# Kernel tuning notes

Measured on AMD Instinct MI355X. Metric: run time of the kernel, lower is better.

The kernel has to match this reference:

```python
import jax, jax.numpy as jnp
import numpy as np

B, N, C_IN = 4, 4096, 64
DIM = 64
NKP = 15
K = 32               # neighbor_limits
CONV_RADIUS = 0.1 * 2.0   # conv_radius * rigid_scale (is_deform=False)
KERNEL_RADIUS = 0.12
RECEP = 1.2          # kernel_point_receptive_radius
TRANS_DIM = 128
INF = 1000000.0


def _square_distance(src, dst):
    # src [B,N,3], dst [B,M,3] -> [B,N,M]
    d = -2.0 * jnp.einsum('bnc,bmc->bnm', src, dst)
    d = d + jnp.sum(src * src, -1)[:, :, None]
    d = d + jnp.sum(dst * dst, -1)[:, None, :]
    return d


def _query_ball(xyz, radius):
    # xyz [B,N,3] -> neighbor idx [B,N,K]; out-of-radius mapped to N (shadow)
    n = xyz.shape[1]
    sq = _square_distance(xyz, xyz)
    idx = jnp.broadcast_to(jnp.arange(n, dtype=jnp.int32), sq.shape)
    idx = jnp.where(sq > radius * radius, n, idx)
    idx = jnp.sort(idx, axis=-1)[:, :, :K]
    return idx


def _index_points(points_bcn, idx, pad_val):
    # points [B,C,N], idx [B,N,K] -> [B,N,K,C]; index N hits shadow row = pad_val
    p = jnp.transpose(points_bcn, (0, 2, 1))          # [B,N,C]
    shadow = jnp.full((p.shape[0], 1, p.shape[2]), pad_val, p.dtype)
    p = jnp.concatenate([p, shadow], axis=1)          # [B,N+1,C]
    b_idx = jnp.arange(p.shape[0])[:, None, None]
    return p[b_idx, idx]                              # [B,N,K,C]


def setup_inputs() -> dict:
    key = jax.random.key(0)
    ks = jax.random.split(key, 12)
    pos = jax.random.uniform(ks[0], (B, 3, N), dtype=jnp.float32)
    feat = jax.random.normal(ks[1], (B, C_IN, N), dtype=jnp.float32)
    # kernel points: center point at origin, rest inside kernel_radius ball ('center' mode)
    kp_rest = jax.random.uniform(ks[2], (3, NKP - 1), minval=-KERNEL_RADIUS,
                                 maxval=KERNEL_RADIUS, dtype=jnp.float32)
    kp_pos = jnp.concatenate([jnp.zeros((3, 1), jnp.float32), kp_rest], axis=1)  # [3,NKP]
    s = 0.05
    cb_w = jax.random.normal(ks[3], (DIM, C_IN), jnp.float32) * s
    cb_b = jax.random.normal(ks[4], (DIM,), jnp.float32) * s
    kp_weight = jax.random.normal(ks[5], (NKP, DIM, DIM), jnp.float32) * s
    kp_bias = jax.random.normal(ks[6], (DIM,), jnp.float32) * s
    ce_w = jax.random.normal(ks[7], (C_IN, DIM), jnp.float32) * s
    ce_b = jax.random.normal(ks[8], (C_IN,), jnp.float32) * s
    f1_w = jax.random.normal(ks[9], (2 * DIM, 2 * DIM), jnp.float32) * s
    f1_b = jnp.zeros((2 * DIM,), jnp.float32)
    f2_w = jax.random.normal(ks[10], (TRANS_DIM, 2 * DIM), jnp.float32) * s
    f2_b = jnp.zeros((TRANS_DIM,), jnp.float32)
    return dict(pos=pos, feat=feat, kp_pos=kp_pos, cb_w=cb_w, cb_b=cb_b,
                kp_weight=kp_weight, kp_bias=kp_bias, ce_w=ce_w, ce_b=ce_b,
                f1_w=f1_w, f1_b=f1_b, f2_w=f2_w, f2_b=f2_b)


def reference(pos, feat, kp_pos, cb_w, cb_b, kp_weight, kp_bias, ce_w, ce_b,
              f1_w, f1_b, f2_w, f2_b):
    xyz = jnp.transpose(jax.lax.stop_gradient(pos), (0, 2, 1))       # [B,N,3]
    neighbor_idx = _query_ball(xyz, CONV_RADIUS)                     # [B,N,K]
    # NOTE: with is_deform=False the original code does NOT subtract the center
    # position; rel_neighbor_pos is the absolute gathered positions.
    neighbor_pos = jnp.transpose(_index_points(pos, neighbor_idx, INF),
                                 (0, 3, 1, 2))                        # [B,3,N,K]
    feat0 = jnp.einsum('oc,bcn->bon', cb_w, feat) + cb_b[None, :, None]
    neighbor_feat = _index_points(feat0, neighbor_idx, 0.0)           # [B,N,K,DIM]

    kp_pos_deform = kp_pos.reshape(1, 3, 1, NKP) + 0.0                # offset = 0
    diff = neighbor_pos[..., None] - kp_pos_deform[:, :, :, None, :]  # [B,3,N,K,NKP]
    sq_d = jnp.sum(diff * diff, axis=1)                               # [B,N,K,NKP]
    w = jnp.clip(1.0 - jnp.sqrt(sq_d) / RECEP, 0.0)                   # [B,N,K,NKP]
    w = jnp.transpose(w, (0, 1, 3, 2))                                # [B,N,NKP,K]
    weighted = jnp.einsum('bnpk,bnkc->bnpc', w, neighbor_feat)        # [B,N,NKP,DIM]
    out = jnp.einsum('bnpc,pcd->bnd', weighted, kp_weight) + kp_bias  # [B,N,DIM]
    out = jax.nn.relu(jnp.transpose(out, (0, 2, 1)))                  # [B,DIM,N]
    out = jax.nn.relu(jnp.einsum('oc,bcn->bon', ce_w, out)
                      + ce_b[None, :, None] + feat)                   # [B,C_IN,N]

    fuse_in = jnp.concatenate(
        [jnp.transpose(weighted, (0, 3, 1, 2)),                       # [B,DIM,N,NKP]
         jnp.broadcast_to(out[..., None], (B, DIM, N, NKP))], axis=1) # [B,2DIM,N,NKP]
    h = jax.nn.relu(jnp.einsum('oc,bcnk->bonk', f1_w, fuse_in)
                    + f1_b[None, :, None, None])
    fuse = jax.nn.relu(jnp.einsum('oc,bcnk->bonk', f2_w, h)
                       + f2_b[None, :, None, None])                   # [B,TRANS_DIM,N,NKP]
    return out, kp_pos_deform, fuse
```

## Files before the change

kernel.cpp:

```cpp
#include <hip/hip_runtime.h>
#include <hip/hip_bf16.h>
#include <stdint.h>

#define NPTS 4096
#define NB   4
#define KNN  32
#define NKPT 15

#define OFF_IDX      0ULL
#define OFF_FEAT0    2097152ULL
#define OFF_WEIGHTED 6292480ULL
#define OFF_ROUT0    37749760ULL
#define OFF_W1P      41944064ULL
#define OFF_W2P      41976832ULL
#define OFF_KPWP     42009600ULL

#define OUT_OFF_OUT  0
#define OUT_OFF_KP   1048576
#define OUT_OFF_FUSE 1048621

#define SBU(u) ((u) ^ (((u) >> 3) & 7))

typedef __attribute__((ext_vector_type(8))) short short8v;
typedef __attribute__((ext_vector_type(4))) float f32x4;

__device__ __forceinline__ unsigned short bf16b(float f) {
  __hip_bfloat16 h = __float2bfloat16(f);
  return *(unsigned short*)&h;
}
__device__ __forceinline__ unsigned pkbf(float lo, float hi) {
  return (unsigned)bf16b(lo) | ((unsigned)bf16b(hi) << 16);
}

__global__ __launch_bounds__(256) void k0_init(const float* __restrict__ f1_w,
                                               const float* __restrict__ f2_w,
                                               const float* __restrict__ kpw,
                                               const float* __restrict__ kp_pos,
                                               unsigned short* __restrict__ w1p,
                                               unsigned short* __restrict__ w2p,
                                               unsigned short* __restrict__ kpwp,
                                               float* __restrict__ feat0,
                                               float* __restrict__ out_kp) {
  int t = blockIdx.x * 256 + threadIdx.x;
  if (t < 32768) {
    const int w = t >> 14;
    const int i = t & 16383;
    const int j = i & 7, l = (i >> 3) & 63, kc = (i >> 9) & 3, ot = i >> 11;
    const int o = ot * 16 + (l & 15);
    const int k = kc * 32 + (l >> 4) * 8 + j;
    const float* src = w ? f2_w : f1_w;
    unsigned short* dst = w ? w2p : w1p;
    dst[i] = bf16b(src[o * 128 + k]);
    return;
  }
  t -= 32768;
  if (t < 61440) {
    const int j = t & 7, l = (t >> 3) & 63, nt = (t >> 9) & 3, kc = t >> 11;
    const int k = kc * 32 + (l >> 4) * 8 + j;
    const int d = nt * 16 + (l & 15);
    kpwp[t] = bf16b(kpw[(size_t)k * 64 + d]);
    return;
  }
  t -= 61440;
  if (t < NB * 64) { int b = t >> 6, d = t & 63; feat0[((size_t)b * (NPTS + 1) + NPTS) * 64 + d] = 0.f; return; }
  t -= NB * 64;
  if (t < 45) out_kp[t] = kp_pos[t];
}

__global__ __launch_bounds__(256) void k1_neigh(const float* __restrict__ pos,
                                                int* __restrict__ idx_ws) {
  const int w = threadIdx.x >> 6, lane = threadIdx.x & 63;
  const int pt = blockIdx.x * 4 + w;
  const int b = pt >> 12, n = pt & 4095;
  const float* px = pos + (size_t)b * 3 * NPTS;
  const double x0 = (double)px[n], y0 = (double)px[NPTS + n], z0 = (double)px[2 * NPTS + n];
  const double ssrc = x0 * x0 + y0 * y0 + z0 * z0;
  const double RAD = 0.1 * 2.0;
  const double R2 = RAD * RAD;
  int cnt = 0;
  int* op = idx_ws + (size_t)pt * KNN;
  for (int ch = 0; ch < 64; ++ch) {
    const int j = ch * 64 + lane;
    const double xj = (double)px[j], yj = (double)px[NPTS + j], zj = (double)px[2 * NPTS + j];
    const double dot  = x0 * xj + y0 * yj + z0 * zj;
    const double sdst = xj * xj + yj * yj + zj * zj;
    const double sq = -2.0 * dot + ssrc + sdst;
    const bool keep = !(sq > R2);
    const unsigned long long m = __ballot(keep);
    if (keep) {
      const int p = cnt + (int)__popcll(m & ((1ULL << lane) - 1ULL));
      if (p < KNN) op[p] = j;
    }
    cnt += (int)__popcll(m);
    if (cnt >= KNN) break;
  }
  const int s = cnt + lane;
  if (s < KNN) op[s] = NPTS;
}

__global__ __launch_bounds__(256) void k2_feat0(const float* __restrict__ feat,
                                                const float* __restrict__ cb_w,
                                                const float* __restrict__ cb_b,
                                                float* __restrict__ feat0) {
  __shared__ float cbt[64 * 65];
  const int t = threadIdx.x;
  #pragma unroll
  for (int q = 0; q < 16; ++q) {
    const int idx = q * 256 + t;
    const int d = idx >> 6, c = idx & 63;
    cbt[c * 65 + d] = cb_w[idx];
  }
  __syncthreads();
  const int ptl = t >> 6, d = t & 63;
  const int pt = blockIdx.x * 4 + ptl;
  const int b = pt >> 12, n = pt & 4095;
  const float* fp = feat + (size_t)b * 64 * NPTS + n;
  float acc = 0.f;
  #pragma unroll
  for (int c = 0; c < 64; ++c) acc = fmaf(cbt[c * 65 + d], fp[(size_t)c * NPTS], acc);
  acc += cb_b[d];
  feat0[((size_t)b * (NPTS + 1) + n) * 64 + d] = acc;
}

__global__ __launch_bounds__(64) void k3_weighted(const float* __restrict__ pos,
                                                  const int* __restrict__ idx_ws,
                                                  const float* __restrict__ feat0,
                                                  const float* __restrict__ kp_pos,
                                                  unsigned short* __restrict__ wbf) {
  __shared__ int   nidx[KNN];
  __shared__ float npx[KNN], npy[KNN], npz[KNN];
  __shared__ float kp[48];
  __shared__ float wl[KNN * 16];
  const int lane = threadIdx.x;
  const int pt = blockIdx.x;
  const int b = pt >> 12;
  if (lane < 45) kp[lane] = kp_pos[lane];
  if (lane < KNN) {
    const int ki = idx_ws[(size_t)pt * KNN + lane];
    nidx[lane] = ki;
    const bool v = ki < NPTS;
    const float* px = pos + (size_t)b * 3 * NPTS;
    npx[lane] = v ? px[ki] : 1000000.0f;
    npy[lane] = v ? px[NPTS + ki] : 1000000.0f;
    npz[lane] = v ? px[2 * NPTS + ki] : 1000000.0f;
  }
  __syncthreads();
  #pragma unroll
  for (int r = 0; r < 8; ++r) {
    const int i = r * 64 + lane;
    const int k = i >> 4, p = i & 15;
    float wv = 0.f;
    if (p < 15) {
      const float dx = npx[k] - kp[p];
      const float dy = npy[k] - kp[15 + p];
      const float dz = npz[k] - kp[30 + p];
      const float d2 = dx * dx + dy * dy + dz * dz;
      wv = fmaxf(1.0f - sqrtf(d2) / 1.2f, 0.f);
    }
    wl[i] = wv;
  }
  __syncthreads();
  float acc[16];
  #pragma unroll
  for (int p = 0; p < 16; ++p) acc[p] = 0.f;
  const float* f0 = feat0 + (size_t)b * (NPTS + 1) * 64 + lane;
  for (int k = 0; k < KNN; ++k) {
    const float f = f0[(size_t)nidx[k] * 64];
    #pragma unroll
    for (int q = 0; q < 4; ++q) {
      const float4 w4 = *(const float4*)&wl[k * 16 + q * 4];
      acc[q * 4 + 0] = fmaf(w4.x, f, acc[q * 4 + 0]);
      acc[q * 4 + 1] = fmaf(w4.y, f, acc[q * 4 + 1]);
      acc[q * 4 + 2] = fmaf(w4.z, f, acc[q * 4 + 2]);
      acc[q * 4 + 3] = fmaf(w4.w, f, acc[q * 4 + 3]);
    }
  }
  unsigned short* wp = wbf + (size_t)pt * NKPT * 64 + lane;
  #pragma unroll
  for (int p = 0; p < 15; ++p) wp[(size_t)p * 64] = bf16b(acc[p]);
}

__global__ __launch_bounds__(64) void k4_kpconv(const unsigned short* __restrict__ wbf,
                                                const unsigned short* __restrict__ kpwp,
                                                const float* __restrict__ kp_bias,
                                                float* __restrict__ rout0) {
  const int lane = threadIdx.x;
  const int m0 = blockIdx.x * 16;
  const short8v* kf = (const short8v*)kpwp;
  f32x4 acc[4];
  #pragma unroll
  for (int nt = 0; nt < 4; ++nt) acc[nt] = (f32x4){0.f, 0.f, 0.f, 0.f};
  const unsigned short* ap = wbf + (size_t)(m0 + (lane & 15)) * 960 + (lane >> 4) * 8;
  #pragma unroll 6
  for (int kc = 0; kc < 30; ++kc) {
    const short8v a = *(const short8v*)&ap[kc * 32];
    #pragma unroll
    for (int nt = 0; nt < 4; ++nt)
      acc[nt] = __builtin_amdgcn_mfma_f32_16x16x32_bf16(a, kf[(kc * 4 + nt) * 64 + lane], acc[nt], 0, 0, 0);
  }
  const int row = m0 + (lane >> 4) * 4;
  #pragma unroll
  for (int nt = 0; nt < 4; ++nt) {
    const int d = nt * 16 + (lane & 15);
    const float bv = kp_bias[d];
    #pragma unroll
    for (int r = 0; r < 4; ++r)
      rout0[(size_t)(row + r) * 64 + d] = fmaxf(acc[nt][r] + bv, 0.f);
  }
}

__global__ __launch_bounds__(256) void k5_out(const float* __restrict__ rout0,
                                              const float* __restrict__ ce_w,
                                              const float* __restrict__ ce_b,
                                              const float* __restrict__ feat,
                                              float* __restrict__ out) {
  __shared__ float r0[64 * 65];
  __shared__ float cwt[64 * 64];
  const int t = threadIdx.x;
  const int b = blockIdx.x >> 6;
  const int n0 = (blockIdx.x & 63) * 64;
  #pragma unroll
  for (int q = 0; q < 16; ++q) {
    const int idx = q * 256 + t;
    const int rr = idx >> 6, c = idx & 63;
    r0[rr * 65 + c] = rout0[((size_t)b * 4096 + n0 + rr) * 64 + c];
    cwt[idx] = ce_w[(idx & 63) * 64 + (idx >> 6)];
  }
  __syncthreads();
  const int nl = t & 63, og = t >> 6;
  float acc[16];
  #pragma unroll
  for (int j = 0; j < 16; ++j) acc[j] = 0.f;
  for (int c = 0; c < 64; ++c) {
    const float x = r0[nl * 65 + c];
    #pragma unroll
    for (int q = 0; q < 4; ++q) {
      const float4 w4 = *(const float4*)&cwt[c * 64 + og * 16 + q * 4];
      acc[q * 4 + 0] = fmaf(w4.x, x, acc[q * 4 + 0]);
      acc[q * 4 + 1] = fmaf(w4.y, x, acc[q * 4 + 1]);
      acc[q * 4 + 2] = fmaf(w4.z, x, acc[q * 4 + 2]);
      acc[q * 4 + 3] = fmaf(w4.w, x, acc[q * 4 + 3]);
    }
  }
  #pragma unroll
  for (int q = 0; q < 4; ++q) {
    const float4 cb4 = *(const float4*)&ce_b[og * 16 + q * 4];
    const float cbv[4] = {cb4.x, cb4.y, cb4.z, cb4.w};
    #pragma unroll
    for (int j = 0; j < 4; ++j) {
      const int o = og * 16 + q * 4 + j;
      const float fv = feat[((size_t)b * 64 + o) * 4096 + n0 + nl];
      out[((size_t)b * 64 + o) * 4096 + n0 + nl] = fmaxf((acc[q * 4 + j] + cbv[j]) + fv, 0.f);
    }
  }
}

__global__ __launch_bounds__(256, 2) void k6_fuse(const unsigned short* __restrict__ wbf,
                                                  const float* __restrict__ outp,
                                                  const unsigned short* __restrict__ w1p,
                                                  const float* __restrict__ f1_b,
                                                  const unsigned short* __restrict__ w2p,
                                                  const float* __restrict__ f2_b,
                                                  float* __restrict__ fuse) {
  __shared__ __attribute__((aligned(16))) unsigned short SB[16384];
  __shared__ float outS[64 * 12];
  const int t = threadIdx.x;
  const int blk = blockIdx.x;
  const int b = blk / 480;
  const int ml0 = (blk - b * 480) * 128;
  const size_t M0 = (size_t)blk * 128;
  const int wv = t >> 6, lane = t & 63;
  const short8v* w1f = (const short8v*)w1p;
  const short8v* w2f = (const short8v*)w2p;

  short8v w1r[32];
  #pragma unroll
  for (int i = 0; i < 32; ++i) w1r[i] = w1f[i * 64 + lane];

  const int nmin = ml0 / 15;
  #pragma unroll
  for (int q = 0; q < 3; ++q) {
    const int i = q * 256 + t;
    const int c2 = i / 12, nn = i - c2 * 12;
    int n = nmin + nn;
    if (n > 4095) n = 4095;
    outS[i] = outp[((size_t)b * 64 + c2) * 4096 + n];
  }
  #pragma unroll
  for (int q = 0; q < 4; ++q) {
    const int chunk = q * 256 + t;
    const int m = chunk >> 3, a = chunk & 7;
    const uint4 pk = *(const uint4*)&wbf[(M0 + m) * 64 + a * 8];
    const int kc = a >> 2, hi = a & 3;
    const int u = ((m >> 4) * 4 + kc) * 64 + hi * 16 + (m & 15);
    *(uint4*)&SB[SBU(u) * 8] = pk;
  }
  __syncthreads();
  #pragma unroll
  for (int q = 0; q < 4; ++q) {
    const int chunk = q * 256 + t;
    const int m = chunk >> 3, a = chunk & 7;
    const int dn = (ml0 + m) / 15 - nmin;
    float v[8];
    #pragma unroll
    for (int i = 0; i < 8; ++i) v[i] = outS[(a * 8 + i) * 12 + dn];
    const int c0 = 64 + a * 8;
    const int kc = c0 >> 5, hi = (c0 >> 3) & 3;
    const int u = ((m >> 4) * 4 + kc) * 64 + hi * 16 + (m & 15);
    uint4 pk;
    pk.x = pkbf(v[0], v[1]); pk.y = pkbf(v[2], v[3]);
    pk.z = pkbf(v[4], v[5]); pk.w = pkbf(v[6], v[7]);
    *(uint4*)&SB[SBU(u) * 8] = pk;
  }
  __syncthreads();

  short8v xf[8];
  #pragma unroll
  for (int mt = 0; mt < 2; ++mt)
    #pragma unroll
    for (int kc = 0; kc < 4; ++kc) {
      const int u = ((wv * 2 + mt) * 4 + kc) * 64 + lane;
      xf[mt * 4 + kc] = *(const short8v*)&SB[SBU(u) * 8];
    }

  f32x4 acc[8][2];
  #pragma unroll
  for (int ot = 0; ot < 8; ++ot) {
    acc[ot][0] = (f32x4){0.f, 0.f, 0.f, 0.f};
    acc[ot][1] = (f32x4){0.f, 0.f, 0.f, 0.f};
  }
  #pragma unroll
  for (int kc = 0; kc < 4; ++kc) {
    #pragma unroll
    for (int ot = 0; ot < 8; ++ot) {
      acc[ot][0] = __builtin_amdgcn_mfma_f32_16x16x32_bf16(w1r[ot * 4 + kc], xf[kc],     acc[ot][0], 0, 0, 0);
      acc[ot][1] = __builtin_amdgcn_mfma_f32_16x16x32_bf16(w1r[ot * 4 + kc], xf[4 + kc], acc[ot][1], 0, 0, 0);
    }
  }
  short8v w2r[32];
  #pragma unroll
  for (int i = 0; i < 32; ++i) w2r[i] = w2f[i * 64 + lane];

  const int rb = (lane >> 4) * 4;
  #pragma unroll
  for (int ot = 0; ot < 8; ++ot) {
    const int o0 = ot * 16 + rb;
    const float4 b1 = *(const float4*)&f1_b[o0];
    const int kc = o0 >> 5, hi = (o0 >> 3) & 3, j0 = o0 & 7;
    #pragma unroll
    for (int mt = 0; mt < 2; ++mt) {
      const f32x4 h = acc[ot][mt];
      const float h0 = fmaxf(h[0] + b1.x, 0.f);
      const float h1 = fmaxf(h[1] + b1.y, 0.f);
      const float h2 = fmaxf(h[2] + b1.z, 0.f);
      const float h3 = fmaxf(h[3] + b1.w, 0.f);
      const int u = ((wv * 2 + mt) * 4 + kc) * 64 + hi * 16 + (lane & 15);
      uint2 pk;
      pk.x = pkbf(h0, h1);
      pk.y = pkbf(h2, h3);
      *(uint2*)&SB[SBU(u) * 8 + j0] = pk;
    }
  }
  short8v hf[8];
  #pragma unroll
  for (int mt = 0; mt < 2; ++mt)
    #pragma unroll
    for (int kc = 0; kc < 4; ++kc) {
      const int u = ((wv * 2 + mt) * 4 + kc) * 64 + lane;
      hf[mt * 4 + kc] = *(const short8v*)&SB[SBU(u) * 8];
    }
  #pragma unroll
  for (int ot = 0; ot < 8; ++ot) {
    acc[ot][0] = (f32x4){0.f, 0.f, 0.f, 0.f};
    acc[ot][1] = (f32x4){0.f, 0.f, 0.f, 0.f};
  }
  #pragma unroll
  for (int kc = 0; kc < 4; ++kc) {
    #pragma unroll
    for (int ot = 0; ot < 8; ++ot) {
      acc[ot][0] = __builtin_amdgcn_mfma_f32_16x16x32_bf16(w2r[ot * 4 + kc], hf[kc],     acc[ot][0], 0, 0, 0);
      acc[ot][1] = __builtin_amdgcn_mfma_f32_16x16x32_bf16(w2r[ot * 4 + kc], hf[4 + kc], acc[ot][1], 0, 0, 0);
    }
  }
  float* fp0 = fuse + (size_t)b * 128 * 61440 + ml0 + wv * 32 + (lane & 15);
  #pragma unroll
  for (int ot = 0; ot < 8; ++ot) {
    const int o0 = ot * 16 + rb;
    const float4 b2 = *(const float4*)&f2_b[o0];
    const float bv[4] = {b2.x, b2.y, b2.z, b2.w};
    #pragma unroll
    for (int mt = 0; mt < 2; ++mt) {
      const f32x4 vacc = acc[ot][mt];
      #pragma unroll
      for (int r = 0; r < 4; ++r)
        fp0[(size_t)(o0 + r) * 61440 + mt * 16] = fmaxf(vacc[r] + bv[r], 0.f);
    }
  }
}

extern "C" void kernel_launch(void* const* d_in, const int* in_sizes, int n_in,
                              void* d_out, int out_size, void* d_ws, size_t ws_size,
                              hipStream_t stream) {
  const float* pos     = (const float*)d_in[0];
  const float* feat    = (const float*)d_in[1];
  const float* kp_pos  = (const float*)d_in[2];
  const float* cb_w    = (const float*)d_in[3];
  const float* cb_b    = (const float*)d_in[4];
  const float* kpw     = (const float*)d_in[5];
  const float* kp_bias = (const float*)d_in[6];
  const float* ce_w    = (const float*)d_in[7];
  const float* ce_b    = (const float*)d_in[8];
  const float* f1_w    = (const float*)d_in[9];
  const float* f1_b    = (const float*)d_in[10];
  const float* f2_w    = (const float*)d_in[11];
  const float* f2_b    = (const float*)d_in[12];
  float* out = (float*)d_out;
  char* ws = (char*)d_ws;
  int*   idx_ws   = (int*)(ws + OFF_IDX);
  float* feat0    = (float*)(ws + OFF_FEAT0);
  unsigned short* wbf  = (unsigned short*)(ws + OFF_WEIGHTED);
  float* rout0    = (float*)(ws + OFF_ROUT0);
  unsigned short* w1p  = (unsigned short*)(ws + OFF_W1P);
  unsigned short* w2p  = (unsigned short*)(ws + OFF_W2P);
  unsigned short* kpwp = (unsigned short*)(ws + OFF_KPWP);

  k0_init<<<370, 256, 0, stream>>>(f1_w, f2_w, kpw, kp_pos, w1p, w2p, kpwp, feat0,
                                   out + OUT_OFF_KP);
  k1_neigh<<<4096, 256, 0, stream>>>(pos, idx_ws);
  k2_feat0<<<4096, 256, 0, stream>>>(feat, cb_w, cb_b, feat0);
  k3_weighted<<<16384, 64, 0, stream>>>(pos, idx_ws, feat0, kp_pos, wbf);
  k4_kpconv<<<1024, 64, 0, stream>>>(wbf, kpwp, kp_bias, rout0);
  k5_out<<<256, 256, 0, stream>>>(rout0, ce_w, ce_b, feat, out + OUT_OFF_OUT);
  k6_fuse<<<1920, 256, 0, stream>>>(wbf, out + OUT_OFF_OUT, w1p, f1_b, w2p, f2_b,
                                    out + OUT_OFF_FUSE);
}
```

Baseline: 156.5 us.

## Merge setup kernels, fuse kpconv with output, precompute broadcast half of fuse MLP

```diff
diff --git a/kernel.cpp b/kernel.cpp
--- a/kernel.cpp
+++ b/kernel.cpp
@@ -10,10 +10,10 @@
 #define OFF_IDX      0ULL
 #define OFF_FEAT0    2097152ULL
 #define OFF_WEIGHTED 6292480ULL
-#define OFF_ROUT0    37749760ULL
-#define OFF_W1P      41944064ULL
-#define OFF_W2P      41976832ULL
-#define OFF_KPWP     42009600ULL
+#define OFF_HO       37749760ULL
+#define OFF_W1P      46138368ULL
+#define OFF_W2P      46171136ULL
+#define OFF_KPWP     46203904ULL
 
 #define OUT_OFF_OUT  0
 #define OUT_OFF_KP   1048576
@@ -32,16 +32,73 @@
   return (unsigned)bf16b(lo) | ((unsigned)bf16b(hi) << 16);
 }
 
-__global__ __launch_bounds__(256) void k0_init(const float* __restrict__ f1_w,
-                                               const float* __restrict__ f2_w,
-                                               const float* __restrict__ kpw,
-                                               const float* __restrict__ kp_pos,
-                                               unsigned short* __restrict__ w1p,
-                                               unsigned short* __restrict__ w2p,
-                                               unsigned short* __restrict__ kpwp,
-                                               float* __restrict__ feat0,
-                                               float* __restrict__ out_kp) {
-  int t = blockIdx.x * 256 + threadIdx.x;
+__global__ __launch_bounds__(256) void k012(const float* __restrict__ pos,
+                                            const float* __restrict__ feat,
+                                            const float* __restrict__ cb_w,
+                                            const float* __restrict__ cb_b,
+                                            const float* __restrict__ f1_w,
+                                            const float* __restrict__ f2_w,
+                                            const float* __restrict__ kpw,
+                                            const float* __restrict__ kp_pos,
+                                            int* __restrict__ idx_ws,
+                                            float* __restrict__ feat0,
+                                            unsigned short* __restrict__ w1p,
+                                            unsigned short* __restrict__ w2p,
+                                            unsigned short* __restrict__ kpwp,
+                                            float* __restrict__ out_kp) {
+  __shared__ float cbt[64 * 65];
+  const int blk = blockIdx.x;
+  if (blk < 4096) {
+    const int w = threadIdx.x >> 6, lane = threadIdx.x & 63;
+    const int pt = blk * 4 + w;
+    const int b = pt >> 12, n = pt & 4095;
+    const float* px = pos + (size_t)b * 3 * NPTS;
+    const double x0 = (double)px[n], y0 = (double)px[NPTS + n], z0 = (double)px[2 * NPTS + n];
+    const double ssrc = x0 * x0 + y0 * y0 + z0 * z0;
+    const double RAD = 0.1 * 2.0;
+    const double R2 = RAD * RAD;
+    int cnt = 0;
+    int* op = idx_ws + (size_t)pt * KNN;
+    for (int ch = 0; ch < 64; ++ch) {
+      const int j = ch * 64 + lane;
+      const double xj = (double)px[j], yj = (double)px[NPTS + j], zj = (double)px[2 * NPTS + j];
+      const double dot  = x0 * xj + y0 * yj + z0 * zj;
+      const double sdst = xj * xj + yj * yj + zj * zj;
+      const double sq = -2.0 * dot + ssrc + sdst;
+      const bool keep = !(sq > R2);
+      const unsigned long long m = __ballot(keep);
+      if (keep) {
+        const int p = cnt + (int)__popcll(m & ((1ULL << lane) - 1ULL));
+        if (p < KNN) op[p] = j;
+      }
+      cnt += (int)__popcll(m);
+      if (cnt >= KNN) break;
+    }
+    const int s = cnt + lane;
+    if (s < KNN) op[s] = NPTS;
+    return;
+  }
+  if (blk < 8192) {
+    const int t = threadIdx.x;
+    #pragma unroll
+    for (int q = 0; q < 16; ++q) {
+      const int idx = q * 256 + t;
+      const int d = idx >> 6, c = idx & 63;
+      cbt[c * 65 + d] = cb_w[idx];
+    }
+    __syncthreads();
+    const int ptl = t >> 6, d = t & 63;
+    const int pt = (blk - 4096) * 4 + ptl;
+    const int b = pt >> 12, n = pt & 4095;
+    const float* fp = feat + (size_t)b * 64 * NPTS + n;
+    float acc = 0.f;
+    #pragma unroll
+    for (int c = 0; c < 64; ++c) acc = fmaf(cbt[c * 65 + d], fp[(size_t)c * NPTS], acc);
+    acc += cb_b[d];
+    feat0[((size_t)b * (NPTS + 1) + n) * 64 + d] = acc;
+    return;
+  }
+  int t = (blk - 8192) * 256 + threadIdx.x;
   if (t < 32768) {
     const int w = t >> 14;
     const int i = t & 16383;
@@ -65,61 +122,6 @@
   if (t < NB * 64) { int b = t >> 6, d = t & 63; feat0[((size_t)b * (NPTS + 1) + NPTS) * 64 + d] = 0.f; return; }
   t -= NB * 64;
   if (t < 45) out_kp[t] = kp_pos[t];
-}
-
-__global__ __launch_bounds__(256) void k1_neigh(const float* __restrict__ pos,
-                                                int* __restrict__ idx_ws) {
-  const int w = threadIdx.x >> 6, lane = threadIdx.x & 63;
-  const int pt = blockIdx.x * 4 + w;
-  const int b = pt >> 12, n = pt & 4095;
-  const float* px = pos + (size_t)b * 3 * NPTS;
-  const double x0 = (double)px[n], y0 = (double)px[NPTS + n], z0 = (double)px[2 * NPTS + n];
-  const double ssrc = x0 * x0 + y0 * y0 + z0 * z0;
-  const double RAD = 0.1 * 2.0;
-  const double R2 = RAD * RAD;
-  int cnt = 0;
-  int* op = idx_ws + (size_t)pt * KNN;
-  for (int ch = 0; ch < 64; ++ch) {
-    const int j = ch * 64 + lane;
-    const double xj = (double)px[j], yj = (double)px[NPTS + j], zj = (double)px[2 * NPTS + j];
-    const double dot  = x0 * xj + y0 * yj + z0 * zj;
-    const double sdst = xj * xj + yj * yj + zj * zj;
-    const double sq = -2.0 * dot + ssrc + sdst;
-    const bool keep = !(sq > R2);
-    const unsigned long long m = __ballot(keep);
-    if (keep) {
-      const int p = cnt + (int)__popcll(m & ((1ULL << lane) - 1ULL));
-      if (p < KNN) op[p] = j;
-    }
-    cnt += (int)__popcll(m);
-    if (cnt >= KNN) break;
-  }
-  const int s = cnt + lane;
-  if (s < KNN) op[s] = NPTS;
-}
-
-__global__ __launch_bounds__(256) void k2_feat0(const float* __restrict__ feat,
-                                                const float* __restrict__ cb_w,
-                                                const float* __restrict__ cb_b,
-                                                float* __restrict__ feat0) {
-  __shared__ float cbt[64 * 65];
-  const int t = threadIdx.x;
-  #pragma unroll
-  for (int q = 0; q < 16; ++q) {
-    const int idx = q * 256 + t;
-    const int d = idx >> 6, c = idx & 63;
-    cbt[c * 65 + d] = cb_w[idx];
-  }
-  __syncthreads();
-  const int ptl = t >> 6, d = t & 63;
-  const int pt = blockIdx.x * 4 + ptl;
-  const int b = pt >> 12, n = pt & 4095;
-  const float* fp = feat + (size_t)b * 64 * NPTS + n;
-  float acc = 0.f;
-  #pragma unroll
-  for (int c = 0; c < 64; ++c) acc = fmaf(cbt[c * 65 + d], fp[(size_t)c * NPTS], acc);
-  acc += cb_b[d];
-  feat0[((size_t)b * (NPTS + 1) + n) * 64 + d] = acc;
 }
 
 __global__ __launch_bounds__(64) void k3_weighted(const float* __restrict__ pos,
@@ -180,16 +182,33 @@
   for (int p = 0; p < 15; ++p) wp[(size_t)p * 64] = bf16b(acc[p]);
 }
 
-__global__ __launch_bounds__(64) void k4_kpconv(const unsigned short* __restrict__ wbf,
-                                                const unsigned short* __restrict__ kpwp,
-                                                const float* __restrict__ kp_bias,
-                                                float* __restrict__ rout0) {
-  const int lane = threadIdx.x;
-  const int m0 = blockIdx.x * 16;
+__global__ __launch_bounds__(256) void k45(const unsigned short* __restrict__ wbf,
+                                           const unsigned short* __restrict__ kpwp,
+                                           const float* __restrict__ kp_bias,
+                                           const float* __restrict__ ce_w,
+                                           const float* __restrict__ ce_b,
+                                           const float* __restrict__ feat,
+                                           const unsigned short* __restrict__ w1p,
+                                           const float* __restrict__ f1_b,
+                                           float* __restrict__ out,
+                                           float* __restrict__ hO) {
+  __shared__ float r0[64 * 65];
+  __shared__ float cwt[64 * 64];
+  __shared__ unsigned short outT[64 * 74];
+  const int t = threadIdx.x;
+  const int b = blockIdx.x >> 6;
+  const int n0 = (blockIdx.x & 63) * 64;
+  const int wv = t >> 6, lane = t & 63;
+  #pragma unroll
+  for (int q = 0; q < 16; ++q) {
+    const int idx = q * 256 + t;
+    cwt[idx] = ce_w[(idx & 63) * 64 + (idx >> 6)];
+  }
   const short8v* kf = (const short8v*)kpwp;
   f32x4 acc[4];
   #pragma unroll
   for (int nt = 0; nt < 4; ++nt) acc[nt] = (f32x4){0.f, 0.f, 0.f, 0.f};
+  const int m0 = b * 4096 + n0 + wv * 16;
   const unsigned short* ap = wbf + (size_t)(m0 + (lane & 15)) * 960 + (lane >> 4) * 8;
   #pragma unroll 6
   for (int kc = 0; kc < 30; ++kc) {
@@ -198,48 +217,29 @@
     for (int nt = 0; nt < 4; ++nt)
       acc[nt] = __builtin_amdgcn_mfma_f32_16x16x32_bf16(a, kf[(kc * 4 + nt) * 64 + lane], acc[nt], 0, 0, 0);
   }
-  const int row = m0 + (lane >> 4) * 4;
+  const int rl = wv * 16 + (lane >> 4) * 4;
   #pragma unroll
   for (int nt = 0; nt < 4; ++nt) {
     const int d = nt * 16 + (lane & 15);
     const float bv = kp_bias[d];
     #pragma unroll
     for (int r = 0; r < 4; ++r)
-      rout0[(size_t)(row + r) * 64 + d] = fmaxf(acc[nt][r] + bv, 0.f);
-  }
-}
-
-__global__ __launch_bounds__(256) void k5_out(const float* __restrict__ rout0,
-                                              const float* __restrict__ ce_w,
-                                              const float* __restrict__ ce_b,
-                                              const float* __restrict__ feat,
-                                              float* __restrict__ out) {
-  __shared__ float r0[64 * 65];
-  __shared__ float cwt[64 * 64];
-  const int t = threadIdx.x;
-  const int b = blockIdx.x >> 6;
-  const int n0 = (blockIdx.x & 63) * 64;
-  #pragma unroll
-  for (int q = 0; q < 16; ++q) {
-    const int idx = q * 256 + t;
-    const int rr = idx >> 6, c = idx & 63;
-    r0[rr * 65 + c] = rout0[((size_t)b * 4096 + n0 + rr) * 64 + c];
-    cwt[idx] = ce_w[(idx & 63) * 64 + (idx >> 6)];
+      r0[(rl + r) * 65 + d] = fmaxf(acc[nt][r] + bv, 0.f);
   }
   __syncthreads();
   const int nl = t & 63, og = t >> 6;
-  float acc[16];
-  #pragma unroll
-  for (int j = 0; j < 16; ++j) acc[j] = 0.f;
+  float facc[16];
+  #pragma unroll
+  for (int j = 0; j < 16; ++j) facc[j] = 0.f;
   for (int c = 0; c < 64; ++c) {
     const float x = r0[nl * 65 + c];
     #pragma unroll
     for (int q = 0; q < 4; ++q) {
       const float4 w4 = *(const float4*)&cwt[c * 64 + og * 16 + q * 4];
-      acc[q * 4 + 0] = fmaf(w4.x, x, acc[q * 4 + 0]);
-      acc[q * 4 + 1] = fmaf(w4.y, x, acc[q * 4 + 1]);
-      acc[q * 4 + 2] = fmaf(w4.z, x, acc[q * 4 + 2]);
-      acc[q * 4 + 3] = fmaf(w4.w, x, acc[q * 4 + 3]);
+      facc[q * 4 + 0] = fmaf(w4.x, x, facc[q * 4 + 0]);
+      facc[q * 4 + 1] = fmaf(w4.y, x, facc[q * 4 + 1]);
+      facc[q * 4 + 2] = fmaf(w4.z, x, facc[q * 4 + 2]);
+      facc[q * 4 + 3] = fmaf(w4.w, x, facc[q * 4 + 3]);
     }
   }
   #pragma unroll
@@ -250,20 +250,47 @@
     for (int j = 0; j < 4; ++j) {
       const int o = og * 16 + q * 4 + j;
       const float fv = feat[((size_t)b * 64 + o) * 4096 + n0 + nl];
-      out[((size_t)b * 64 + o) * 4096 + n0 + nl] = fmaxf((acc[q * 4 + j] + cbv[j]) + fv, 0.f);
-    }
+      const float v = fmaxf((facc[q * 4 + j] + cbv[j]) + fv, 0.f);
+      out[((size_t)b * 64 + o) * 4096 + n0 + nl] = v;
+      outT[o * 74 + nl] = bf16b(v);
+    }
+  }
+  __syncthreads();
+  const short8v* w1f = (const short8v*)w1p;
+  f32x4 hacc[8];
+  #pragma unroll
+  for (int ot = 0; ot < 8; ++ot) hacc[ot] = (f32x4){0.f, 0.f, 0.f, 0.f};
+  const int nw = lane & 15;
+  #pragma unroll
+  for (int kc2 = 0; kc2 < 2; ++kc2) {
+    short8v bfr;
+    #pragma unroll
+    for (int j = 0; j < 8; ++j)
+      bfr[j] = (short)outT[(kc2 * 32 + (lane >> 4) * 8 + j) * 74 + wv * 16 + nw];
+    #pragma unroll
+    for (int ot = 0; ot < 8; ++ot)
+      hacc[ot] = __builtin_amdgcn_mfma_f32_16x16x32_bf16(w1f[(ot * 4 + 2 + kc2) * 64 + lane], bfr, hacc[ot], 0, 0, 0);
+  }
+  const int rb = (lane >> 4) * 4;
+  float* hp = hO + ((size_t)b * 4096 + n0 + wv * 16 + nw) * 128;
+  #pragma unroll
+  for (int ot = 0; ot < 8; ++ot) {
+    const float4 b1 = *(const float4*)&f1_b[ot * 16 + rb];
+    const float bv[4] = {b1.x, b1.y, b1.z, b1.w};
+    #pragma unroll
+    for (int r = 0; r < 4; ++r)
+      hp[ot * 16 + rb + r] = hacc[ot][r] + bv[r];
   }
 }
 
 __global__ __launch_bounds__(256, 2) void k6_fuse(const unsigned short* __restrict__ wbf,
-                                                  const float* __restrict__ outp,
+                                                  const float* __restrict__ hO,
                                                   const unsigned short* __restrict__ w1p,
-                                                  const float* __restrict__ f1_b,
                                                   const unsigned short* __restrict__ w2p,
                                                   const float* __restrict__ f2_b,
                                                   float* __restrict__ fuse) {
   __shared__ __attribute__((aligned(16))) unsigned short SB[16384];
-  __shared__ float outS[64 * 12];
+  __shared__ __attribute__((aligned(16))) float hOS[12 * 128];
   const int t = threadIdx.x;
   const int blk = blockIdx.x;
   const int b = blk / 480;
@@ -273,19 +300,13 @@
   const short8v* w1f = (const short8v*)w1p;
   const short8v* w2f = (const short8v*)w2p;
 
-  short8v w1r[32];
-  #pragma unroll
-  for (int i = 0; i < 32; ++i) w1r[i] = w1f[i * 64 + lane];
-
-  const int nmin = ml0 / 15;
-  #pragma unroll
-  for (int q = 0; q < 3; ++q) {
-    const int i = q * 256 + t;
-    const int c2 = i / 12, nn = i - c2 * 12;
-    int n = nmin + nn;
-    if (n > 4095) n = 4095;
-    outS[i] = outp[((size_t)b * 64 + c2) * 4096 + n];
-  }
+  short8v w1r[16];
+  #pragma unroll
+  for (int ot = 0; ot < 8; ++ot)
+    #pragma unroll
+    for (int kc = 0; kc < 2; ++kc)
+      w1r[ot * 2 + kc] = w1f[(ot * 4 + kc) * 64 + lane];
+
   #pragma unroll
   for (int q = 0; q < 4; ++q) {
     const int chunk = q * 256 + t;
@@ -295,65 +316,58 @@
     const int u = ((m >> 4) * 4 + kc) * 64 + hi * 16 + (m & 15);
     *(uint4*)&SB[SBU(u) * 8] = pk;
   }
+  const int nmin = ml0 / 15;
+  #pragma unroll
+  for (int q = 0; q < 6; ++q) {
+    const int idx = q * 256 + t;
+    const int row = idx >> 7, o = idx & 127;
+    int n = nmin + row;
+    if (n > 4095) n = 4095;
+    hOS[idx] = hO[((size_t)b * 4096 + n) * 128 + o];
+  }
   __syncthreads();
-  #pragma unroll
-  for (int q = 0; q < 4; ++q) {
-    const int chunk = q * 256 + t;
-    const int m = chunk >> 3, a = chunk & 7;
-    const int dn = (ml0 + m) / 15 - nmin;
-    float v[8];
-    #pragma unroll
-    for (int i = 0; i < 8; ++i) v[i] = outS[(a * 8 + i) * 12 + dn];
-    const int c0 = 64 + a * 8;
-    const int kc = c0 >> 5, hi = (c0 >> 3) & 3;
-    const int u = ((m >> 4) * 4 + kc) * 64 + hi * 16 + (m & 15);
-    uint4 pk;
-    pk.x = pkbf(v[0], v[1]); pk.y = pkbf(v[2], v[3]);
-    pk.z = pkbf(v[4], v[5]); pk.w = pkbf(v[6], v[7]);
-    *(uint4*)&SB[SBU(u) * 8] = pk;
-  }
-  __syncthreads();
-
-  short8v xf[8];
+
+  short8v xf[4];
   #pragma unroll
   for (int mt = 0; mt < 2; ++mt)
     #pragma unroll
-    for (int kc = 0; kc < 4; ++kc) {
+    for (int kc = 0; kc < 2; ++kc) {
       const int u = ((wv * 2 + mt) * 4 + kc) * 64 + lane;
-      xf[mt * 4 + kc] = *(const short8v*)&SB[SBU(u) * 8];
-    }
-
+      xf[mt * 2 + kc] = *(const short8v*)&SB[SBU(u) * 8];
+    }
+
+  const int rb = (lane >> 4) * 4;
+  const int dnA = (ml0 + wv * 32 + (lane & 15)) / 15 - nmin;
+  const int dnB = (ml0 + wv * 32 + 16 + (lane & 15)) / 15 - nmin;
   f32x4 acc[8][2];
   #pragma unroll
   for (int ot = 0; ot < 8; ++ot) {
-    acc[ot][0] = (f32x4){0.f, 0.f, 0.f, 0.f};
-    acc[ot][1] = (f32x4){0.f, 0.f, 0.f, 0.f};
-  }
-  #pragma unroll
-  for (int kc = 0; kc < 4; ++kc) {
+    acc[ot][0] = *(const f32x4*)&hOS[dnA * 128 + ot * 16 + rb];
+    acc[ot][1] = *(const f32x4*)&hOS[dnB * 128 + ot * 16 + rb];
+  }
+  #pragma unroll
+  for (int kc = 0; kc < 2; ++kc) {
     #pragma unroll
     for (int ot = 0; ot < 8; ++ot) {
-      acc[ot][0] = __builtin_amdgcn_mfma_f32_16x16x32_bf16(w1r[ot * 4 + kc], xf[kc],     acc[ot][0], 0, 0, 0);
-      acc[ot][1] = __builtin_amdgcn_mfma_f32_16x16x32_bf16(w1r[ot * 4 + kc], xf[4 + kc], acc[ot][1], 0, 0, 0);
+      acc[ot][0] = __builtin_amdgcn_mfma_f32_16x16x32_bf16(w1r[ot * 2 + kc], xf[kc],     acc[ot][0], 0, 0, 0);
+      acc[ot][1] = __builtin_amdgcn_mfma_f32_16x16x32_bf16(w1r[ot * 2 + kc], xf[2 + kc], acc[ot][1], 0, 0, 0);
     }
   }
   short8v w2r[32];
   #pragma unroll
   for (int i = 0; i < 32; ++i) w2r[i] = w2f[i * 64 + lane];
 
-  const int rb = (lane >> 4) * 4;
   #pragma unroll
   for (int ot = 0; ot < 8; ++ot) {
     const int o0 = ot * 16 + rb;
-    const float4 b1 = *(const float4*)&f1_b[o0];
     const int kc = o0 >> 5, hi = (o0 >> 3) & 3, j0 = o0 & 7;
     #pragma unroll
     for (int mt = 0; mt < 2; ++mt) {
       const f32x4 h = acc[ot][mt];
-      const float h0 = fmaxf(h[0] + b1.x, 0.f);
-      const float h1 = fmaxf(h[1] + b1.y, 0.f);
-      const float h2 = fmaxf(h[2] + b1.z, 0.f);
-      const float h3 = fmaxf(h[3] + b1.w, 0.f);
+      const float h0 = fmaxf(h[0], 0.f);
+      const float h1 = fmaxf(h[1], 0.f);
+      const float h2 = fmaxf(h[2], 0.f);
+      const float h3 = fmaxf(h[3], 0.f);
       const int u = ((wv * 2 + mt) * 4 + kc) * 64 + hi * 16 + (lane & 15);
       uint2 pk;
       pk.x = pkbf(h0, h1);
@@ -419,18 +433,15 @@
   int*   idx_ws   = (int*)(ws + OFF_IDX);
   float* feat0    = (float*)(ws + OFF_FEAT0);
   unsigned short* wbf  = (unsigned short*)(ws + OFF_WEIGHTED);
-  float* rout0    = (float*)(ws + OFF_ROUT0);
+  float* hO       = (float*)(ws + OFF_HO);
   unsigned short* w1p  = (unsigned short*)(ws + OFF_W1P);
   unsigned short* w2p  = (unsigned short*)(ws + OFF_W2P);
   unsigned short* kpwp = (unsigned short*)(ws + OFF_KPWP);
 
-  k0_init<<<370, 256, 0, stream>>>(f1_w, f2_w, kpw, kp_pos, w1p, w2p, kpwp, feat0,
-                                   out + OUT_OFF_KP);
-  k1_neigh<<<4096, 256, 0, stream>>>(pos, idx_ws);
-  k2_feat0<<<4096, 256, 0, stream>>>(feat, cb_w, cb_b, feat0);
+  k012<<<8562, 256, 0, stream>>>(pos, feat, cb_w, cb_b, f1_w, f2_w, kpw, kp_pos,
+                                 idx_ws, feat0, w1p, w2p, kpwp, out + OUT_OFF_KP);
   k3_weighted<<<16384, 64, 0, stream>>>(pos, idx_ws, feat0, kp_pos, wbf);
-  k4_kpconv<<<1024, 64, 0, stream>>>(wbf, kpwp, kp_bias, rout0);
-  k5_out<<<256, 256, 0, stream>>>(rout0, ce_w, ce_b, feat, out + OUT_OFF_OUT);
-  k6_fuse<<<1920, 256, 0, stream>>>(wbf, out + OUT_OFF_OUT, w1p, f1_b, w2p, f2_b,
-                                    out + OUT_OFF_FUSE);
-}
+  k45<<<256, 256, 0, stream>>>(wbf, kpwp, kp_bias, ce_w, ce_b, feat, w1p, f1_b,
+                               out + OUT_OFF_OUT, hO);
+  k6_fuse<<<1920, 256, 0, stream>>>(wbf, hO, w1p, w2p, f2_b, out + OUT_OFF_FUSE);
+}
```

New measurement: 134.2 us. 14.2% less time.
